# Optimization experiments

Hardware: AMD Instinct MI355X
Metric: run time of the kernel (lower is better)

The kernel has to match this reference:

```python
import jax, jax.numpy as jnp
import numpy as np

N_EMBD = 2048
EPS = 1e-5

def layernorm(x, g, b):
    mu = jnp.mean(x, axis=-1, keepdims=True)
    var = jnp.mean(jnp.square(x - mu), axis=-1, keepdims=True)
    return (x - mu) * jax.lax.rsqrt(var + EPS) * g + b

def gelu_erf(x):
    return x * 0.5 * (1.0 + jax.lax.erf(x / jnp.sqrt(jnp.asarray(2.0, x.dtype))))

def setup_inputs() -> dict:
    key = jax.random.key(0)
    ks = jax.random.split(key, 2)
    x = jax.random.normal(ks[0], (4, 4096, N_EMBD), dtype=jnp.float32)
    W = jax.random.normal(ks[1], (N_EMBD, N_EMBD), dtype=jnp.float32) / np.sqrt(N_EMBD)
    bW = jnp.zeros((N_EMBD,), jnp.float32)
    g1 = jnp.ones((N_EMBD,), jnp.float32)
    b1 = jnp.zeros((N_EMBD,), jnp.float32)
    g2 = jnp.ones((N_EMBD,), jnp.float32)
    b2 = jnp.zeros((N_EMBD,), jnp.float32)
    return {"x": x, "W": W, "bW": bW, "g1": g1, "b1": b1, "g2": g2, "b2": b2}

def reference(x, W, bW, g1, b1, g2, b2):
    h = layernorm(x, g1, b1)                         # [B,S,D]
    h = jnp.einsum('bsd,ed->bse', h, W) + bW         # Linear(D,D)
    h = gelu_erf(h)
    return layernorm(h, g2, b2)
```

## Files before the change

kernel.cpp:

```cpp
#include <hip/hip_runtime.h>
#include <hip/hip_bf16.h>
#include <math.h>


#define D 2048
#define MROWS 16384
#define BMT 256
#define BNT 256
#define KTILES (D / 64)

typedef __bf16 bf16x8 __attribute__((ext_vector_type(8)));
typedef float f32x4 __attribute__((ext_vector_type(4)));

#define GLP(p) ((const __attribute__((address_space(1))) void*)(p))
#define LDSP(p) ((__attribute__((address_space(3))) void*)(p))
#define S_VMCNT(n) asm volatile("s_waitcnt vmcnt(" #n ")" ::: "memory")
#define MEMFENCE() asm volatile("" ::: "memory")
#define BAR() __builtin_amdgcn_s_barrier()
#define SCHED_FENCE() __builtin_amdgcn_sched_barrier(0)

__device__ __forceinline__ float gelu_f(float v) {
  return 0.5f * v * (1.0f + erff(v * 0.70710678118654752f));
}

__global__ __launch_bounds__(256) void ln1_kernel(
    const float* __restrict__ x, const float* __restrict__ g,
    const float* __restrict__ b, __hip_bfloat16* __restrict__ out) {
  const int tid = threadIdx.x;
  const size_t row = blockIdx.x;
  const float4* xr = (const float4*)(x + row * D);
  float4 v0 = xr[2 * tid];
  float4 v1 = xr[2 * tid + 1];
  float s  = v0.x + v0.y + v0.z + v0.w + v1.x + v1.y + v1.z + v1.w;
  float ss = v0.x*v0.x + v0.y*v0.y + v0.z*v0.z + v0.w*v0.w
           + v1.x*v1.x + v1.y*v1.y + v1.z*v1.z + v1.w*v1.w;
#pragma unroll
  for (int off = 32; off > 0; off >>= 1) {
    s  += __shfl_down(s, off, 64);
    ss += __shfl_down(ss, off, 64);
  }
  __shared__ float red[8];
  const int w = tid >> 6;
  if ((tid & 63) == 0) { red[w] = s; red[w + 4] = ss; }
  __syncthreads();
  s  = red[0] + red[1] + red[2] + red[3];
  ss = red[4] + red[5] + red[6] + red[7];
  const float mu  = s * (1.0f / D);
  const float var = ss * (1.0f / D) - mu * mu;
  const float inv = rsqrtf(var + 1e-5f);
  const float4* gv = (const float4*)g;
  const float4* bv = (const float4*)b;
  float4 g0 = gv[2 * tid], g1 = gv[2 * tid + 1];
  float4 b0 = bv[2 * tid], b1 = bv[2 * tid + 1];
  alignas(16) __hip_bfloat16 h[8];
  h[0] = __float2bfloat16((v0.x - mu) * inv * g0.x + b0.x);
  h[1] = __float2bfloat16((v0.y - mu) * inv * g0.y + b0.y);
  h[2] = __float2bfloat16((v0.z - mu) * inv * g0.z + b0.z);
  h[3] = __float2bfloat16((v0.w - mu) * inv * g0.w + b0.w);
  h[4] = __float2bfloat16((v1.x - mu) * inv * g1.x + b1.x);
  h[5] = __float2bfloat16((v1.y - mu) * inv * g1.y + b1.y);
  h[6] = __float2bfloat16((v1.z - mu) * inv * g1.z + b1.z);
  h[7] = __float2bfloat16((v1.w - mu) * inv * g1.w + b1.w);
  *(uint4*)(out + row * D + (size_t)tid * 8) = *(const uint4*)h;
}

__global__ __launch_bounds__(256) void cvt_kernel(
    const float* __restrict__ W, __hip_bfloat16* __restrict__ Wb, int n8) {
  const int i = blockIdx.x * 256 + threadIdx.x;
  if (i >= n8) return;
  const float4* p = (const float4*)W + 2 * (size_t)i;
  float4 a = p[0], c = p[1];
  alignas(16) __hip_bfloat16 h[8] = {
      __float2bfloat16(a.x), __float2bfloat16(a.y),
      __float2bfloat16(a.z), __float2bfloat16(a.w),
      __float2bfloat16(c.x), __float2bfloat16(c.y),
      __float2bfloat16(c.z), __float2bfloat16(c.w)};
  *(uint4*)(Wb + (size_t)i * 8) = *(const uint4*)h;
}

template <bool BFO>
__global__ __launch_bounds__(512, 2) void gemm_kernel(
    const __hip_bfloat16* __restrict__ A,
    const __hip_bfloat16* __restrict__ Bw,
    const float* __restrict__ bias,
    void* __restrict__ Cout) {
  __shared__ __hip_bfloat16 sA[2 * 2 * 256 * 32];
  __shared__ __hip_bfloat16 sB[2 * 2 * 256 * 32];
  const int tid = threadIdx.x;
  const int l = tid & 63;
  const int wid = tid >> 6;
  const int fr = l & 15;
  const int lk = l >> 4;
  const size_t m0 = (size_t)blockIdx.x * BMT;
  const int n0 = blockIdx.y * BNT;
  const int whm = wid >> 2;
  const int wn = (wid & 3) * 64;

  const int slot = ((2 * lk + (fr & 1)) ^ (fr >> 1)) << 4;
  const int aoff = whm * 8192 + (fr >> 1) * 128 + slot;
  const int boff = wn * 64 + (fr >> 1) * 128 + slot;

  const int line = tid >> 3;
  const int v = (tid & 7) ^ (line & 7);
  const int srow0 = 2 * line + (v & 1);
  const int srow1 = srow0 + 128;
  const int scol = (v >> 1) * 8;
  const int ldd0 = tid * 16;
  const int ldd1 = ldd0 + 8192;
  const __hip_bfloat16* const Ag = A + m0 * D;
  const __hip_bfloat16* const Bg = Bw + (size_t)n0 * D;

  auto stg = [&](const __hip_bfloat16* G, char* lds, int so, int kh, int kt) {
    const __hip_bfloat16* s0 = G + (size_t)srow0 * D + kt * 64 + kh * 32 + scol;
    const __hip_bfloat16* s1 = G + (size_t)srow1 * D + kt * 64 + kh * 32 + scol;
    char* q = lds + (so << 15) + (kh << 14);
    __builtin_amdgcn_global_load_lds(GLP(s0), LDSP(q + ldd0), 16, 0, 0);
    __builtin_amdgcn_global_load_lds(GLP(s1), LDSP(q + ldd1), 16, 0, 0);
  };

  bf16x8 a[8], b[4];
  f32x4 acc[8][4] = {};

  auto rd = [&](int bo, int kh) {
    const char* pa = (const char*)sA + bo + (kh << 14) + aoff;
    const char* pb = (const char*)sB + bo + (kh << 14) + boff;
#pragma unroll
    for (int mi = 0; mi < 8; ++mi) a[mi] = *(const bf16x8*)(pa + mi * 1024);
#pragma unroll
    for (int ni = 0; ni < 4; ++ni) b[ni] = *(const bf16x8*)(pb + ni * 1024);
  };
  auto mma = [&]() {
    __builtin_amdgcn_s_setprio(1);
#pragma unroll
    for (int mi = 0; mi < 8; ++mi)
#pragma unroll
      for (int ni = 0; ni < 4; ++ni)
        acc[mi][ni] = __builtin_amdgcn_mfma_f32_16x16x32_bf16(a[mi], b[ni], acc[mi][ni], 0, 0, 0);
    __builtin_amdgcn_s_setprio(0);
  };

  stg(Ag, (char*)sA, 0, 0, 0); stg(Bg, (char*)sB, 0, 0, 0);
  stg(Ag, (char*)sA, 0, 1, 0); stg(Bg, (char*)sB, 0, 1, 0);

  for (int kt = 0; kt < KTILES - 1; ++kt) {
    const int bo = (kt & 1) << 15;
    const int so = (kt & 1) ^ 1;
    S_VMCNT(4);
    BAR(); MEMFENCE(); SCHED_FENCE();
    rd(bo, 0);
    stg(Ag, (char*)sA, so, 0, kt + 1); stg(Bg, (char*)sB, so, 0, kt + 1);
    mma();
    S_VMCNT(4);
    BAR(); MEMFENCE(); SCHED_FENCE();
    rd(bo, 1);
    stg(Ag, (char*)sA, so, 1, kt + 1); stg(Bg, (char*)sB, so, 1, kt + 1);
    mma();
  }
  {
    const int bo = ((KTILES - 1) & 1) << 15;
    S_VMCNT(4);
    BAR(); MEMFENCE(); SCHED_FENCE();
    rd(bo, 0);
    mma();
    S_VMCNT(0);
    BAR(); MEMFENCE(); SCHED_FENCE();
    rd(bo, 1);
    mma();
  }

  float bv[4];
#pragma unroll
  for (int ni = 0; ni < 4; ++ni) bv[ni] = bias[n0 + wn + ni * 16 + fr];
#pragma unroll
  for (int mi = 0; mi < 8; ++mi) {
    const size_t rbase = m0 + whm * 128 + mi * 16 + lk * 4;
#pragma unroll
    for (int rr = 0; rr < 4; ++rr) {
      const size_t ro = (rbase + rr) * D + n0 + wn + fr;
#pragma unroll
      for (int ni = 0; ni < 4; ++ni) {
        const float val = gelu_f(acc[mi][ni][rr] + bv[ni]);
        if constexpr (BFO)
          ((__hip_bfloat16*)Cout)[ro + ni * 16] = __float2bfloat16(val);
        else
          ((float*)Cout)[ro + ni * 16] = val;
      }
    }
  }
}

__global__ __launch_bounds__(256) void ln2_kernel(
    float* __restrict__ C, const float* __restrict__ g, const float* __restrict__ b) {
  const int tid = threadIdx.x;
  const size_t row = blockIdx.x;
  float4* cr = (float4*)(C + row * D);
  float4 v0 = cr[2 * tid], v1 = cr[2 * tid + 1];
  float s  = v0.x + v0.y + v0.z + v0.w + v1.x + v1.y + v1.z + v1.w;
  float ss = v0.x*v0.x + v0.y*v0.y + v0.z*v0.z + v0.w*v0.w
           + v1.x*v1.x + v1.y*v1.y + v1.z*v1.z + v1.w*v1.w;
#pragma unroll
  for (int off = 32; off > 0; off >>= 1) {
    s  += __shfl_down(s, off, 64);
    ss += __shfl_down(ss, off, 64);
  }
  __shared__ float red[8];
  const int w = tid >> 6;
  if ((tid & 63) == 0) { red[w] = s; red[w + 4] = ss; }
  __syncthreads();
  s  = red[0] + red[1] + red[2] + red[3];
  ss = red[4] + red[5] + red[6] + red[7];
  const float mu  = s * (1.0f / D);
  const float var = ss * (1.0f / D) - mu * mu;
  const float inv = rsqrtf(var + 1e-5f);
  const float4* gv = (const float4*)g;
  const float4* bv = (const float4*)b;
  float4 g0 = gv[2 * tid], g1 = gv[2 * tid + 1];
  float4 b0 = bv[2 * tid], b1 = bv[2 * tid + 1];
  float4 o0, o1;
  o0.x = (v0.x - mu) * inv * g0.x + b0.x;
  o0.y = (v0.y - mu) * inv * g0.y + b0.y;
  o0.z = (v0.z - mu) * inv * g0.z + b0.z;
  o0.w = (v0.w - mu) * inv * g0.w + b0.w;
  o1.x = (v1.x - mu) * inv * g1.x + b1.x;
  o1.y = (v1.y - mu) * inv * g1.y + b1.y;
  o1.z = (v1.z - mu) * inv * g1.z + b1.z;
  o1.w = (v1.w - mu) * inv * g1.w + b1.w;
  cr[2 * tid] = o0;
  cr[2 * tid + 1] = o1;
}

__global__ __launch_bounds__(256) void ln2b_kernel(
    const __hip_bfloat16* __restrict__ H, const float* __restrict__ g,
    const float* __restrict__ b, float* __restrict__ out) {
  const int tid = threadIdx.x;
  const size_t row = blockIdx.x;
  const uint4 hv = ((const uint4*)(H + row * D))[tid];
  float v[8];
  const unsigned wds[4] = {hv.x, hv.y, hv.z, hv.w};
#pragma unroll
  for (int i = 0; i < 4; ++i) {
    unsigned lo = (wds[i] & 0xffffu) << 16;
    unsigned hi = wds[i] & 0xffff0000u;
    v[2 * i]     = __builtin_bit_cast(float, lo);
    v[2 * i + 1] = __builtin_bit_cast(float, hi);
  }
  float s = 0.f, ss = 0.f;
#pragma unroll
  for (int i = 0; i < 8; ++i) { s += v[i]; ss += v[i] * v[i]; }
#pragma unroll
  for (int off = 32; off > 0; off >>= 1) {
    s  += __shfl_down(s, off, 64);
    ss += __shfl_down(ss, off, 64);
  }
  __shared__ float red[8];
  const int w = tid >> 6;
  if ((tid & 63) == 0) { red[w] = s; red[w + 4] = ss; }
  __syncthreads();
  s  = red[0] + red[1] + red[2] + red[3];
  ss = red[4] + red[5] + red[6] + red[7];
  const float mu  = s * (1.0f / D);
  const float var = ss * (1.0f / D) - mu * mu;
  const float inv = rsqrtf(var + 1e-5f);
  const float4* gv = (const float4*)g;
  const float4* bv = (const float4*)b;
  float4 g0 = gv[2 * tid], g1 = gv[2 * tid + 1];
  float4 b0 = bv[2 * tid], b1 = bv[2 * tid + 1];
  float4 o0, o1;
  o0.x = (v[0] - mu) * inv * g0.x + b0.x;
  o0.y = (v[1] - mu) * inv * g0.y + b0.y;
  o0.z = (v[2] - mu) * inv * g0.z + b0.z;
  o0.w = (v[3] - mu) * inv * g0.w + b0.w;
  o1.x = (v[4] - mu) * inv * g1.x + b1.x;
  o1.y = (v[5] - mu) * inv * g1.y + b1.y;
  o1.z = (v[6] - mu) * inv * g1.z + b1.z;
  o1.w = (v[7] - mu) * inv * g1.w + b1.w;
  float4* orow = (float4*)(out + row * D);
  orow[2 * tid] = o0;
  orow[2 * tid + 1] = o1;
}

extern "C" void kernel_launch(void* const* d_in, const int* in_sizes, int n_in,
                              void* d_out, int out_size, void* d_ws, size_t ws_size,
                              hipStream_t stream) {
  const float* x  = (const float*)d_in[0];
  const float* W  = (const float*)d_in[1];
  const float* bW = (const float*)d_in[2];
  const float* g1 = (const float*)d_in[3];
  const float* b1 = (const float*)d_in[4];
  const float* g2 = (const float*)d_in[5];
  const float* b2 = (const float*)d_in[6];
  float* out = (float*)d_out;

  __hip_bfloat16* Abf = (__hip_bfloat16*)d_ws;
  __hip_bfloat16* Wbf = Abf + (size_t)MROWS * D;
  __hip_bfloat16* H2  = Wbf + (size_t)D * D;
  const size_t need = ((size_t)MROWS * D * 2 + (size_t)D * D) * sizeof(__hip_bfloat16);

  ln1_kernel<<<MROWS, 256, 0, stream>>>(x, g1, b1, Abf);
  cvt_kernel<<<(D * D / 8) / 256, 256, 0, stream>>>(W, Wbf, D * D / 8);
  dim3 grid(MROWS / BMT, D / BNT);
  if (ws_size >= need) {
    gemm_kernel<true><<<grid, 512, 0, stream>>>(Abf, Wbf, bW, (void*)H2);
    ln2b_kernel<<<MROWS, 256, 0, stream>>>(H2, g2, b2, out);
  } else {
    gemm_kernel<false><<<grid, 512, 0, stream>>>(Abf, Wbf, bW, (void*)out);
    ln2_kernel<<<MROWS, 256, 0, stream>>>(out, g2, b2);
  }
}
```

Measured before the change: 229.3 us.

## Restructure GEMM main loop into quadrant-wise 8-wave ping-pong schedule

Reorganizes the bf16 GEMM's shared-memory layout from two K-halves of 32 to M/N halves with a full 64-wide K slice, and splits each K tile into four quadrant MFMA phases. Global-to-LDS staging for the next tiles is interleaved between these phases, with barriers and lgkmcnt waits so that LDS reads, async loads and MFMAs overlap more finely. The aim is to hide load latency and reduce LDS read stalls, at the cost of more barriers and a more fragile schedule with a new swizzle.

```diff
diff --git a/kernel.cpp b/kernel.cpp
--- a/kernel.cpp
+++ b/kernel.cpp
@@ -7,7 +7,7 @@
 #define MROWS 16384
 #define BMT 256
 #define BNT 256
-#define KTILES (D / 64)
+#define KT64 32
 
 typedef __bf16 bf16x8 __attribute__((ext_vector_type(8)));
 typedef float f32x4 __attribute__((ext_vector_type(4)));
@@ -15,6 +15,7 @@
 #define GLP(p) ((const __attribute__((address_space(1))) void*)(p))
 #define LDSP(p) ((__attribute__((address_space(3))) void*)(p))
 #define S_VMCNT(n) asm volatile("s_waitcnt vmcnt(" #n ")" ::: "memory")
+#define S_LGKM0 asm volatile("s_waitcnt lgkmcnt(0)" ::: "memory")
 #define MEMFENCE() asm volatile("" ::: "memory")
 #define BAR() __builtin_amdgcn_s_barrier()
 #define SCHED_FENCE() __builtin_amdgcn_sched_barrier(0)
@@ -84,8 +85,8 @@
     const __hip_bfloat16* __restrict__ Bw,
     const float* __restrict__ bias,
     void* __restrict__ Cout) {
-  __shared__ __hip_bfloat16 sA[2 * 2 * 256 * 32];
-  __shared__ __hip_bfloat16 sB[2 * 2 * 256 * 32];
+  __shared__ __hip_bfloat16 sA[2 * 2 * 128 * 64];
+  __shared__ __hip_bfloat16 sB[2 * 2 * 128 * 64];
   const int tid = threadIdx.x;
   const int l = tid & 63;
   const int wid = tid >> 6;
@@ -95,77 +96,116 @@
   const int n0 = blockIdx.y * BNT;
   const int whm = wid >> 2;
   const int wn = (wid & 3) * 64;
-
-  const int slot = ((2 * lk + (fr & 1)) ^ (fr >> 1)) << 4;
-  const int aoff = whm * 8192 + (fr >> 1) * 128 + slot;
-  const int boff = wn * 64 + (fr >> 1) * 128 + slot;
-
-  const int line = tid >> 3;
-  const int v = (tid & 7) ^ (line & 7);
-  const int srow0 = 2 * line + (v & 1);
-  const int srow1 = srow0 + 128;
-  const int scol = (v >> 1) * 8;
+  const int nhB = wn >> 7;
+
+  const int lk2 = lk ^ (((fr >> 2) & 1) << 1);
+  const int abase = (whm << 14) + fr * 128 + lk2 * 16;
+  const int bbase = (nhB << 14) + ((wn & 64) + fr) * 128 + lk2 * 16;
+
+  const int sline = tid >> 3;
+  const int scn = (tid & 7) ^ (((tid >> 5) & 1) << 1);
   const int ldd0 = tid * 16;
   const int ldd1 = ldd0 + 8192;
-  const __hip_bfloat16* const Ag = A + m0 * D;
-  const __hip_bfloat16* const Bg = Bw + (size_t)n0 * D;
-
-  auto stg = [&](const __hip_bfloat16* G, char* lds, int so, int kh, int kt) {
-    const __hip_bfloat16* s0 = G + (size_t)srow0 * D + kt * 64 + kh * 32 + scol;
-    const __hip_bfloat16* s1 = G + (size_t)srow1 * D + kt * 64 + kh * 32 + scol;
-    char* q = lds + (so << 15) + (kh << 14);
-    __builtin_amdgcn_global_load_lds(GLP(s0), LDSP(q + ldd0), 16, 0, 0);
-    __builtin_amdgcn_global_load_lds(GLP(s1), LDSP(q + ldd1), 16, 0, 0);
-  };
-
-  bf16x8 a[8], b[4];
+
+  auto stgA = [&](int mh, int bufb, int kt) {
+    const __hip_bfloat16* g0 = A + (m0 + mh * 128 + sline) * D + kt * 64 + scn * 8;
+    char* q = (char*)sA + bufb + (mh << 14);
+    __builtin_amdgcn_global_load_lds(GLP(g0), LDSP(q + ldd0), 16, 0, 0);
+    __builtin_amdgcn_global_load_lds(GLP(g0 + (size_t)64 * D), LDSP(q + ldd1), 16, 0, 0);
+  };
+  auto stgB = [&](int nh, int bufb, int kt) {
+    const __hip_bfloat16* g0 = Bw + ((size_t)n0 + nh * 128 + sline) * D + kt * 64 + scn * 8;
+    char* q = (char*)sB + bufb + (nh << 14);
+    __builtin_amdgcn_global_load_lds(GLP(g0), LDSP(q + ldd0), 16, 0, 0);
+    __builtin_amdgcn_global_load_lds(GLP(g0 + (size_t)64 * D), LDSP(q + ldd1), 16, 0, 0);
+  };
+
+  bf16x8 aq[4][2];
+  bf16x8 bq[2][2][2];
   f32x4 acc[8][4] = {};
 
-  auto rd = [&](int bo, int kh) {
-    const char* pa = (const char*)sA + bo + (kh << 14) + aoff;
-    const char* pb = (const char*)sB + bo + (kh << 14) + boff;
-#pragma unroll
-    for (int mi = 0; mi < 8; ++mi) a[mi] = *(const bf16x8*)(pa + mi * 1024);
-#pragma unroll
-    for (int ni = 0; ni < 4; ++ni) b[ni] = *(const bf16x8*)(pb + ni * 1024);
-  };
-  auto mma = [&]() {
+  auto rdA = [&](int mh, int bufb) {
+    const char* p = (const char*)sA + bufb + abase + mh * 8192;
+#pragma unroll
+    for (int mi = 0; mi < 4; ++mi)
+#pragma unroll
+      for (int kk = 0; kk < 2; ++kk)
+        aq[mi][kk] = *(const bf16x8*)(p + mi * 2048 + kk * 64);
+  };
+  auto rdB = [&](int nh, int bufb) {
+    const char* p = (const char*)sB + bufb + bbase + nh * 4096;
+#pragma unroll
+    for (int ni = 0; ni < 2; ++ni)
+#pragma unroll
+      for (int kk = 0; kk < 2; ++kk)
+        bq[nh][ni][kk] = *(const bf16x8*)(p + ni * 2048 + kk * 64);
+  };
+  auto mmaQ = [&](int mh, int nh) {
     __builtin_amdgcn_s_setprio(1);
 #pragma unroll
-    for (int mi = 0; mi < 8; ++mi)
-#pragma unroll
-      for (int ni = 0; ni < 4; ++ni)
-        acc[mi][ni] = __builtin_amdgcn_mfma_f32_16x16x32_bf16(a[mi], b[ni], acc[mi][ni], 0, 0, 0);
+    for (int mi = 0; mi < 4; ++mi)
+#pragma unroll
+      for (int ni = 0; ni < 2; ++ni)
+#pragma unroll
+        for (int kk = 0; kk < 2; ++kk)
+          acc[mh * 4 + mi][nh * 2 + ni] = __builtin_amdgcn_mfma_f32_16x16x32_bf16(
+              aq[mi][kk], bq[nh][ni][kk], acc[mh * 4 + mi][nh * 2 + ni], 0, 0, 0);
     __builtin_amdgcn_s_setprio(0);
   };
 
-  stg(Ag, (char*)sA, 0, 0, 0); stg(Bg, (char*)sB, 0, 0, 0);
-  stg(Ag, (char*)sA, 0, 1, 0); stg(Bg, (char*)sB, 0, 1, 0);
-
-  for (int kt = 0; kt < KTILES - 1; ++kt) {
+  MEMFENCE();
+  stgA(0, 0, 0); stgB(0, 0, 0); stgB(1, 0, 0); stgA(1, 0, 0);
+  stgA(0, 1 << 15, 1); stgB(0, 1 << 15, 1); stgB(1, 1 << 15, 1);
+  MEMFENCE();
+  S_VMCNT(6);
+  BAR(); MEMFENCE(); SCHED_FENCE();
+
+  for (int kt = 0; kt < KT64 - 1; ++kt) {
     const int bo = (kt & 1) << 15;
-    const int so = (kt & 1) ^ 1;
-    S_VMCNT(4);
+    const int bo1 = ((kt + 1) & 1) << 15;
+    const bool st2 = (kt <= KT64 - 3);
+    MEMFENCE();
+    rdA(0, bo); rdB(0, bo);
+    stgA(1, bo1, kt + 1);
+    MEMFENCE(); SCHED_FENCE(); BAR(); MEMFENCE();
+    S_LGKM0; SCHED_FENCE();
+    mmaQ(0, 0);
+    BAR(); MEMFENCE();
+    rdB(1, bo);
+    MEMFENCE(); SCHED_FENCE(); BAR(); MEMFENCE();
+    S_LGKM0; SCHED_FENCE();
+    mmaQ(0, 1);
+    BAR(); MEMFENCE();
+    rdA(1, bo);
+    if (st2) stgB(0, bo, kt + 2);
+    MEMFENCE(); SCHED_FENCE(); BAR(); MEMFENCE();
+    S_LGKM0; SCHED_FENCE();
+    mmaQ(1, 1);
+    BAR(); MEMFENCE();
+    if (st2) { stgB(1, bo, kt + 2); stgA(0, bo, kt + 2); }
+    MEMFENCE();
+    mmaQ(1, 0);
+    if (st2) { S_VMCNT(6); } else { S_VMCNT(0); }
     BAR(); MEMFENCE(); SCHED_FENCE();
-    rd(bo, 0);
-    stg(Ag, (char*)sA, so, 0, kt + 1); stg(Bg, (char*)sB, so, 0, kt + 1);
-    mma();
-    S_VMCNT(4);
-    BAR(); MEMFENCE(); SCHED_FENCE();
-    rd(bo, 1);
-    stg(Ag, (char*)sA, so, 1, kt + 1); stg(Bg, (char*)sB, so, 1, kt + 1);
-    mma();
   }
   {
-    const int bo = ((KTILES - 1) & 1) << 15;
-    S_VMCNT(4);
-    BAR(); MEMFENCE(); SCHED_FENCE();
-    rd(bo, 0);
-    mma();
-    S_VMCNT(0);
-    BAR(); MEMFENCE(); SCHED_FENCE();
-    rd(bo, 1);
-    mma();
+    const int bo = ((KT64 - 1) & 1) << 15;
+    MEMFENCE();
+    rdA(0, bo); rdB(0, bo);
+    MEMFENCE(); SCHED_FENCE(); BAR(); MEMFENCE();
+    S_LGKM0; SCHED_FENCE();
+    mmaQ(0, 0);
+    BAR(); MEMFENCE();
+    rdB(1, bo);
+    MEMFENCE(); SCHED_FENCE(); BAR(); MEMFENCE();
+    S_LGKM0; SCHED_FENCE();
+    mmaQ(0, 1);
+    BAR(); MEMFENCE();
+    rdA(1, bo);
+    MEMFENCE(); SCHED_FENCE(); BAR(); MEMFENCE();
+    S_LGKM0; SCHED_FENCE();
+    mmaQ(1, 1);
+    mmaQ(1, 0);
   }
 
   float bv[4];
```

Measured after the change: 255.6 us. +11.5%, slower.
